# Performance work log

Hardware: AMD Instinct MI355X
Metric: run time of the kernel (lower is better)

## Reference

```python
import jax, jax.numpy as jnp
import numpy as np

B, T, E, H, R = 128, 64, 2048, 1024, 8  # batch, context_window, utter_hidden*2, user_dim, max_roles


def _gru_params(key, in_dim, hid):
    k1, k2, k3, k4 = jax.random.split(key, 4)
    s = 1.0 / np.sqrt(hid)
    return (jax.random.uniform(k1, (3 * hid, in_dim), jnp.float32, -s, s),
            jax.random.uniform(k2, (3 * hid, hid), jnp.float32, -s, s),
            jax.random.uniform(k3, (3 * hid,), jnp.float32, -s, s),
            jax.random.uniform(k4, (3 * hid,), jnp.float32, -s, s))


def setup_inputs() -> dict:
    key = jax.random.key(0)
    ks = jax.random.split(key, 8)
    encoder_hiddens = jax.random.normal(ks[0], (B, T, E), jnp.float32)
    spk = jax.random.randint(ks[1], (B, T), 0, R)
    adr = (spk + jax.random.randint(ks[2], (B, T), 1, R)) % R  # guarantee adr != spk
    dig_users = jnp.stack([spk, adr], axis=-1).astype(jnp.int32)  # [B,T,2]
    ws_ih, ws_hh, ws_bih, ws_bhh = _gru_params(ks[3], E + H, H)  # GRUS: input=[enc; adr_state]
    wa_ih, wa_hh, wa_bih, wa_bhh = _gru_params(ks[4], E + H, H)  # GRUA: input=[enc; spk_state]
    wo_ih, wo_hh, wo_bih, wo_bhh = _gru_params(ks[5], E, H)      # GRUO: input=enc
    return dict(encoder_hiddens=encoder_hiddens, dig_users=dig_users,
                ws_ih=ws_ih, ws_hh=ws_hh, ws_bih=ws_bih, ws_bhh=ws_bhh,
                wa_ih=wa_ih, wa_hh=wa_hh, wa_bih=wa_bih, wa_bhh=wa_bhh,
                wo_ih=wo_ih, wo_hh=wo_hh, wo_bih=wo_bih, wo_bhh=wo_bhh)


def _gru_cell(x, h, w_ih, w_hh, b_ih, b_hh):
    # standard torch.nn.GRUCell math; x: [..., in_dim], h: [..., H]
    gi = x @ w_ih.T + b_ih
    gh = h @ w_hh.T + b_hh
    ir, iz, ig = jnp.split(gi, 3, axis=-1)
    hr, hz, hg = jnp.split(gh, 3, axis=-1)
    r = jax.nn.sigmoid(ir + hr)
    z = jax.nn.sigmoid(iz + hz)
    n = jnp.tanh(ig + r * hg)
    return (1.0 - z) * n + z * h


def reference(encoder_hiddens, dig_users, ws_ih, ws_hh, ws_bih, ws_bhh,
              wa_ih, wa_hh, wa_bih, wa_bhh, wo_ih, wo_hh, wo_bih, wo_bhh):
    bidx = jnp.arange(B)
    roles = jnp.arange(R)

    def step(A, xs):
        enc_t, spk_t, adr_t = xs  # [B,E], [B], [B]
        # others: ascending role indices excluding spk and adr -> [B, R-2]
        is_other = (roles[None, :] != spk_t[:, None]) & (roles[None, :] != adr_t[:, None])
        others = jnp.argsort(jnp.logical_not(is_other).astype(jnp.int32), axis=-1, stable=True)[:, : R - 2]
        # gather current role states (all from pre-update A, as in the original)
        spk_v = A[bidx, spk_t]                    # [B,H]
        adr_v = A[bidx, adr_t]                    # [B,H]
        oth_v = A[bidx[:, None], others]          # [B,R-2,H]
        new_spk = _gru_cell(jnp.concatenate([enc_t, adr_v], -1), spk_v, ws_ih, ws_hh, ws_bih, ws_bhh)
        new_adr = _gru_cell(jnp.concatenate([enc_t, spk_v], -1), adr_v, wa_ih, wa_hh, wa_bih, wa_bhh)
        enc_b = jnp.broadcast_to(enc_t[:, None, :], (B, R - 2, E))
        new_oth = _gru_cell(enc_b, oth_v, wo_ih, wo_hh, wo_bih, wo_bhh)
        # scatter back (spk, adr, others indices are disjoint per batch row)
        A = A.at[bidx, spk_t].set(new_spk)
        A = A.at[bidx, adr_t].set(new_adr)
        A = A.at[bidx[:, None], others].set(new_oth)
        return A, None

    A0 = jnp.zeros((B, R, H), jnp.float32)
    xs = (jnp.swapaxes(encoder_hiddens, 0, 1),  # [T,B,E]
          jnp.swapaxes(dig_users[..., 0], 0, 1),
          jnp.swapaxes(dig_users[..., 1], 0, 1))
    A, _ = jax.lax.scan(step, A0, xs)
    return A
```

## Files before the change

kernel.cpp:

```cpp
#include <hip/hip_runtime.h>
#include <math.h>
#include <stdint.h>

static constexpr int B_ = 128;
static constexpr int T_ = 64;
static constexpr int E_ = 2048;
static constexpr int H_ = 1024;
static constexpr int R_ = 8;
static constexpr int H3_ = 3 * H_;

typedef unsigned short u16;
typedef __attribute__((ext_vector_type(8))) __bf16 bf16x8;
typedef __attribute__((ext_vector_type(4))) float f32x4;

__device__ __forceinline__ u16 f2bf(float f) {
    uint32_t x = __float_as_uint(f);
    x += 0x7fffu + ((x >> 16) & 1u);
    return (u16)(x >> 16);
}
__device__ __forceinline__ float bf2f(u16 u) {
    return __uint_as_float(((uint32_t)u) << 16);
}

__device__ __forceinline__ void async_cp16(const u16* g, u16* l) {
    auto* g1 = (const __attribute__((address_space(1))) u16*)g;
    auto* l3 = (__attribute__((address_space(3))) u16*)(uintptr_t)l;
    __builtin_amdgcn_global_load_lds((const __attribute__((address_space(1))) void*)g1,
                                     (__attribute__((address_space(3))) void*)l3,
                                     16, 0, 0);
}


__global__ __launch_bounds__(256) void zero_kernel(float* __restrict__ p, int n) {
    int i = blockIdx.x * 256 + threadIdx.x;
    if (i < n) p[i] = 0.0f;
}

__global__ __launch_bounds__(256) void conv_bf(
    const float* __restrict__ src, int src_ld, int col0, int cols,
    u16* __restrict__ dst, int total4)
{
    int i4 = blockIdx.x * 256 + threadIdx.x;
    if (i4 >= total4) return;
    int i = i4 * 4;
    int r = i / cols, c = i - r * cols;
    const float4 v = *(const float4*)(src + (size_t)r * src_ld + col0 + c);
    ushort4 o;
    o.x = f2bf(v.x); o.y = f2bf(v.y); o.z = f2bf(v.z); o.w = f2bf(v.w);
    *(ushort4*)(dst + i) = o;
}

__global__ __launch_bounds__(256) void mfma_p1f(
    const u16* __restrict__ X, int t0, int tcshift,
    const u16* __restrict__ W1,
    const float* __restrict__ bs, const float* __restrict__ ba,
    const float* __restrict__ bo,
    u16* __restrict__ GI, size_t GI_elems)
{
    __shared__ u16 As[2][128 * 64];
    __shared__ u16 Bs[2][128 * 64];
    const int tid = threadIdx.x;
    const int which = blockIdx.x / 24;
    const int n0 = (blockIdx.x % 24) * 128;
    const int m0 = blockIdx.y * 128;
    const int tcmask = (1 << tcshift) - 1;

    const u16* W = W1 + (size_t)which * H3_ * E_;
    const float* bias = (which == 0) ? bs : (which == 1) ? ba : bo;
    u16* C = GI + (size_t)which * GI_elems;

    const int lane = tid & 63;
    const int wm = ((tid >> 6) & 1) * 64;
    const int wn = (tid >> 7) * 64;
    const int fr = lane & 15;
    const int kq = (lane >> 4) * 8;
    const int ldsbase = (tid & 192) * 8;

    const int srow = tid >> 3;
    const int sce  = (((tid & 7) * 16) ^ ((srow & 7) << 4)) >> 1;

    f32x4 acc[4][4] = {};

    auto stage = [&](int buf, int k0) {
#pragma unroll
        for (int p = 0; p < 4; ++p) {
            int mrow = m0 + p * 32 + srow;
            int ro = ((mrow >> tcshift) * T_ + t0 + (mrow & tcmask)) * E_;
            async_cp16(X + ro + k0 + sce, &As[buf][p * 2048 + ldsbase]);
            int nrow = n0 + p * 32 + srow;
            async_cp16(W + (size_t)nrow * E_ + k0 + sce, &Bs[buf][p * 2048 + ldsbase]);
        }
    };
    auto compute = [&](int buf) {
#pragma unroll
        for (int kk = 0; kk < 2; ++kk) {
            bf16x8 a[4], b[4];
#pragma unroll
            for (int i = 0; i < 4; ++i) {
                int ra = wm + i * 16 + fr;
                int oa = (ra * 128 + kk * 64 + kq * 2) ^ ((ra & 7) << 4);
                a[i] = *(const bf16x8*)((const char*)&As[buf][0] + oa);
                int rb = wn + i * 16 + fr;
                int ob = (rb * 128 + kk * 64 + kq * 2) ^ ((rb & 7) << 4);
                b[i] = *(const bf16x8*)((const char*)&Bs[buf][0] + ob);
            }
#pragma unroll
            for (int mt = 0; mt < 4; ++mt)
#pragma unroll
                for (int nt = 0; nt < 4; ++nt)
                    acc[mt][nt] = __builtin_amdgcn_mfma_f32_16x16x32_bf16(
                        a[mt], b[nt], acc[mt][nt], 0, 0, 0);
        }
    };

    stage(0, 0);
    __syncthreads();
    int cur = 0;
    for (int k0 = 64; k0 < E_; k0 += 64) {
        stage(cur ^ 1, k0);
        compute(cur);
        __syncthreads();
        cur ^= 1;
    }
    compute(cur);

#pragma unroll
    for (int mt = 0; mt < 4; ++mt)
#pragma unroll
        for (int nt = 0; nt < 4; ++nt) {
            int n = n0 + wn + nt * 16 + fr;
            float bv = bias[n];
#pragma unroll
            for (int i = 0; i < 4; ++i) {
                int m = m0 + wm + mt * 16 + (lane >> 4) * 4 + i;
                C[(size_t)m * H3_ + n] = f2bf(acc[mt][nt][i] + bv);
            }
        }
}

__global__ __launch_bounds__(256) void mfma_step(
    const u16* __restrict__ Abf, const int* __restrict__ dig, int t,
    const u16* __restrict__ Whsi, const u16* __restrict__ Whs,
    const u16* __restrict__ Whai, const u16* __restrict__ Wha,
    const u16* __restrict__ Who, float* __restrict__ G)
{
    __shared__ u16 As[2][64 * 64];
    __shared__ u16 Bs[2][64 * 64];
    __shared__ int rowoff[64];
    const int tid = threadIdx.x;
    const int n0 = blockIdx.x * 64;
    const int row0 = blockIdx.y * 64;

    const u16* W;
    if      (row0 < 128) W = Whsi;
    else if (row0 < 256) W = Whs;
    else if (row0 < 384) W = Whai;
    else if (row0 < 512) W = Wha;
    else                 W = Who;

    if (tid < 64) {
        int mo = row0 + tid;
        int b, role;
        if (mo < 512) {
            b = mo & 127;
            int kind = mo >> 7;
            int spk = dig[(b * T_ + t) * 2 + 0];
            int adr = dig[(b * T_ + t) * 2 + 1];
            role = (kind == 0 || kind == 3) ? adr : spk;
        } else {
            int o = mo - 512;
            b = o / 6;
            int j = o - b * 6;
            int spk = dig[(b * T_ + t) * 2 + 0];
            int adr = dig[(b * T_ + t) * 2 + 1];
            int cnt = 0; role = 0;
            for (int r = 0; r < R_; ++r) {
                if (r != spk && r != adr) {
                    if (cnt == j) { role = r; break; }
                    ++cnt;
                }
            }
        }
        rowoff[tid] = (b * R_ + role) * H_;
    }
    __syncthreads();

    const int lane = tid & 63;
    const int wid = tid >> 6;
    const int wm = (wid & 1) * 32;
    const int wn = (wid >> 1) * 32;
    const int fr = lane & 15;
    const int kq = (lane >> 4) * 8;
    const int ldsbase = (tid & 192) * 8;

    const int srow = tid >> 3;
    const int sce  = (((tid & 7) * 16) ^ ((srow & 7) << 4)) >> 1;

    f32x4 acc[2][2] = {};

    auto stage = [&](int buf, int k0) {
#pragma unroll
        for (int p = 0; p < 2; ++p) {
            int r = p * 32 + srow;
            async_cp16(Abf + rowoff[r] + k0 + sce, &As[buf][p * 2048 + ldsbase]);
            async_cp16(W + (size_t)(n0 + r) * H_ + k0 + sce, &Bs[buf][p * 2048 + ldsbase]);
        }
    };
    auto compute = [&](int buf) {
#pragma unroll
        for (int kk = 0; kk < 2; ++kk) {
            bf16x8 a[2], b[2];
#pragma unroll
            for (int i = 0; i < 2; ++i) {
                int ra = wm + i * 16 + fr;
                int oa = (ra * 128 + kk * 64 + kq * 2) ^ ((ra & 7) << 4);
                a[i] = *(const bf16x8*)((const char*)&As[buf][0] + oa);
                int rb = wn + i * 16 + fr;
                int ob = (rb * 128 + kk * 64 + kq * 2) ^ ((rb & 7) << 4);
                b[i] = *(const bf16x8*)((const char*)&Bs[buf][0] + ob);
            }
#pragma unroll
            for (int mt = 0; mt < 2; ++mt)
#pragma unroll
                for (int nt = 0; nt < 2; ++nt)
                    acc[mt][nt] = __builtin_amdgcn_mfma_f32_16x16x32_bf16(
                        a[mt], b[nt], acc[mt][nt], 0, 0, 0);
        }
    };

    stage(0, 0);
    __syncthreads();
    int cur = 0;
    for (int k0 = 64; k0 < H_; k0 += 64) {
        stage(cur ^ 1, k0);
        compute(cur);
        __syncthreads();
        cur ^= 1;
    }
    compute(cur);

#pragma unroll
    for (int mt = 0; mt < 2; ++mt)
#pragma unroll
        for (int nt = 0; nt < 2; ++nt) {
            int n = n0 + wn + nt * 16 + fr;
#pragma unroll
            for (int i = 0; i < 4; ++i) {
                int mo = row0 + wm + mt * 16 + (lane >> 4) * 4 + i;
                G[(size_t)mo * H3_ + n] = acc[mt][nt][i];
            }
        }
}

__global__ __launch_bounds__(256) void gate_kernel(
    const float* __restrict__ Aold, float* __restrict__ Anew,
    u16* __restrict__ Abf,
    const int* __restrict__ dig, int t, int tloc, int Tc,
    const u16* __restrict__ GIX, const u16* __restrict__ GIA,
    const u16* __restrict__ GIO, const float* __restrict__ G,
    const float* __restrict__ ws_bhh, const float* __restrict__ wa_bhh,
    const float* __restrict__ wo_bhh)
{
    const int blk = blockIdx.x;
    const int b = blk >> 3, r = blk & 7;
    const int spk = dig[(b * T_ + t) * 2 + 0];
    const int adr = dig[(b * T_ + t) * 2 + 1];
    const size_t gi_row = (size_t)(b * Tc + tloc) * H3_;

    const u16* gi_pre;
    const float* gi_add;
    const float* gh;
    const float* bhh;
    if (r == spk) {
        gi_pre = GIX + gi_row;
        gi_add = G + (size_t)b * H3_;
        gh     = G + (size_t)(128 + b) * H3_;
        bhh    = ws_bhh;
    } else if (r == adr) {
        gi_pre = GIA + gi_row;
        gi_add = G + (size_t)(256 + b) * H3_;
        gh     = G + (size_t)(384 + b) * H3_;
        bhh    = wa_bhh;
    } else {
        int oidx = r - (spk < r ? 1 : 0) - (adr < r ? 1 : 0);
        gi_pre = GIO + gi_row;
        gi_add = nullptr;
        gh     = G + (size_t)(512 + b * 6 + oidx) * H3_;
        bhh    = wo_bhh;
    }

    const size_t hoff = (size_t)(b * R_ + r) * H_;
    for (int i = threadIdx.x; i < H_; i += 256) {
        float gir = bf2f(gi_pre[i]);
        float giz = bf2f(gi_pre[H_ + i]);
        float gin = bf2f(gi_pre[2 * H_ + i]);
        if (gi_add) {
            gir += gi_add[i];
            giz += gi_add[H_ + i];
            gin += gi_add[2 * H_ + i];
        }
        float ghr = gh[i]          + bhh[i];
        float ghz = gh[H_ + i]     + bhh[H_ + i];
        float ghn = gh[2 * H_ + i] + bhh[2 * H_ + i];

        float rg = 1.0f / (1.0f + __expf(-(gir + ghr)));
        float zg = 1.0f / (1.0f + __expf(-(giz + ghz)));
        float ng = tanhf(gin + rg * ghn);
        float h  = Aold[hoff + i];
        float o  = (1.0f - zg) * ng + zg * h;
        Anew[hoff + i] = o;
        Abf[hoff + i]  = f2bf(o);
    }
}

extern "C" void kernel_launch(void* const* d_in, const int* in_sizes, int n_in,
                              void* d_out, int out_size, void* d_ws, size_t ws_size,
                              hipStream_t stream) {
    const float* enc    = (const float*)d_in[0];
    const int*   dig    = (const int*)d_in[1];
    const float* ws_ih  = (const float*)d_in[2];
    const float* ws_hh  = (const float*)d_in[3];
    const float* ws_bih = (const float*)d_in[4];
    const float* ws_bhh = (const float*)d_in[5];
    const float* wa_ih  = (const float*)d_in[6];
    const float* wa_hh  = (const float*)d_in[7];
    const float* wa_bih = (const float*)d_in[8];
    const float* wa_bhh = (const float*)d_in[9];
    const float* wo_ih  = (const float*)d_in[10];
    const float* wo_hh  = (const float*)d_in[11];
    const float* wo_bih = (const float*)d_in[12];
    const float* wo_bhh = (const float*)d_in[13];

    float* A0 = (float*)d_out;

    char* p = (char*)d_ws;
    auto take = [&](size_t bytes) { char* q = p; p += (bytes + 255) & ~(size_t)255; return q; };
    u16*   enc_bf = (u16*)  take((size_t)B_ * T_ * E_ * 2);
    u16*   W1     = (u16*)  take((size_t)3 * H3_ * E_ * 2);
    u16*   W1s    = W1;
    u16*   W1a    = W1 + (size_t)H3_ * E_;
    u16*   W1o    = W1a + (size_t)H3_ * E_;
    u16*   Whsi   = (u16*)  take((size_t)H3_ * H_ * 2);
    u16*   Whai   = (u16*)  take((size_t)H3_ * H_ * 2);
    u16*   Whs    = (u16*)  take((size_t)H3_ * H_ * 2);
    u16*   Wha    = (u16*)  take((size_t)H3_ * H_ * 2);
    u16*   Who    = (u16*)  take((size_t)H3_ * H_ * 2);
    u16*   Abf    = (u16*)  take((size_t)B_ * R_ * H_ * 2);
    float* A1     = (float*)take((size_t)B_ * R_ * H_ * 4);
    float* G      = (float*)take((size_t)1280 * H3_ * 4);
    size_t fixed = (size_t)(p - (char*)d_ws);

    const size_t per_t = (size_t)3 * B_ * H3_ * 2;
    int Tc = 64;
    while (Tc > 1 && fixed + per_t * (size_t)Tc > ws_size) Tc >>= 1;
    int tcshift = 0;
    while ((1 << tcshift) < Tc) ++tcshift;
    const size_t GI_elems = (size_t)B_ * Tc * H3_;
    u16* GI  = (u16*)take(3 * GI_elems * 2);
    u16* GIX = GI;
    u16* GIA = GI + GI_elems;
    u16* GIO = GIA + GI_elems;

    dim3 blk(256);
    const size_t A_sz = (size_t)B_ * R_ * H_;

    zero_kernel<<<dim3((int)((A_sz + 255) / 256)), blk, 0, stream>>>(A0, (int)A_sz);
    zero_kernel<<<dim3((int)((A_sz / 2 + 255) / 256)), blk, 0, stream>>>((float*)Abf, (int)(A_sz / 2));

    {
        int t4;
        t4 = B_ * T_ * E_ / 4;
        conv_bf<<<dim3((t4 + 255) / 256), blk, 0, stream>>>(enc, E_, 0, E_, enc_bf, t4);
        t4 = H3_ * E_ / 4;
        conv_bf<<<dim3((t4 + 255) / 256), blk, 0, stream>>>(ws_ih, E_ + H_, 0, E_, W1s, t4);
        conv_bf<<<dim3((t4 + 255) / 256), blk, 0, stream>>>(wa_ih, E_ + H_, 0, E_, W1a, t4);
        conv_bf<<<dim3((t4 + 255) / 256), blk, 0, stream>>>(wo_ih, E_, 0, E_, W1o, t4);
        t4 = H3_ * H_ / 4;
        conv_bf<<<dim3((t4 + 255) / 256), blk, 0, stream>>>(ws_ih, E_ + H_, E_, H_, Whsi, t4);
        conv_bf<<<dim3((t4 + 255) / 256), blk, 0, stream>>>(wa_ih, E_ + H_, E_, H_, Whai, t4);
        conv_bf<<<dim3((t4 + 255) / 256), blk, 0, stream>>>(ws_hh, H_, 0, H_, Whs, t4);
        conv_bf<<<dim3((t4 + 255) / 256), blk, 0, stream>>>(wa_hh, H_, 0, H_, Wha, t4);
        conv_bf<<<dim3((t4 + 255) / 256), blk, 0, stream>>>(wo_hh, H_, 0, H_, Who, t4);
    }

    float* Aold = A0;
    float* Anew = A1;
    for (int t0 = 0; t0 < T_; t0 += Tc) {
        dim3 g1(72, (B_ * Tc) / 128);
        mfma_p1f<<<g1, blk, 0, stream>>>(enc_bf, t0, tcshift, W1,
                                         ws_bih, wa_bih, wo_bih, GI, GI_elems);

        for (int t = t0; t < t0 + Tc; ++t) {
            mfma_step<<<dim3(48, 20), blk, 0, stream>>>(
                Abf, dig, t, Whsi, Whs, Whai, Wha, Who, G);
            gate_kernel<<<dim3(B_ * R_), blk, 0, stream>>>(
                Aold, Anew, Abf, dig, t, t - t0, Tc, GIX, GIA, GIO, G,
                ws_bhh, wa_bhh, wo_bhh);
            float* tmp = Aold; Aold = Anew; Anew = tmp;
        }
    }
}
```

Measured before the change: 2.168 ms.

## Enlarge step GEMM M-tile with XCD-aware block mapping, vectorize gate kernel

The per-step recurrent GEMM now uses 128-row M tiles instead of 64, so each block reuses one loaded weight tile across twice as many rows, and the grid is halved. Blocks are remapped so that blocks sharing the same weight group land on the same XCD, aiming for better L2 locality. The input-projection GEMM swaps grid axes so consecutive blocks share weight tiles, and its bf16 output is written with nontemporal stores. The gate kernel is vectorized to four elements per thread with float4 loads, dropping the strided loop. These add register pressure and rely on H equalling four times the block size.

```diff
diff --git a/kernel.cpp b/kernel.cpp
--- a/kernel.cpp
+++ b/kernel.cpp
@@ -10,6 +10,7 @@
 static constexpr int H3_ = 3 * H_;
 
 typedef unsigned short u16;
+typedef __attribute__((ext_vector_type(4))) unsigned short u16x4;
 typedef __attribute__((ext_vector_type(8))) __bf16 bf16x8;
 typedef __attribute__((ext_vector_type(4))) float f32x4;
 
@@ -60,9 +61,9 @@
     __shared__ u16 As[2][128 * 64];
     __shared__ u16 Bs[2][128 * 64];
     const int tid = threadIdx.x;
-    const int which = blockIdx.x / 24;
-    const int n0 = (blockIdx.x % 24) * 128;
-    const int m0 = blockIdx.y * 128;
+    const int m0 = blockIdx.x * 128;
+    const int which = blockIdx.y / 24;
+    const int n0 = (blockIdx.y % 24) * 128;
     const int tcmask = (1 << tcshift) - 1;
 
     const u16* W = W1 + (size_t)which * H3_ * E_;
@@ -133,7 +134,8 @@
 #pragma unroll
             for (int i = 0; i < 4; ++i) {
                 int m = m0 + wm + mt * 16 + (lane >> 4) * 4 + i;
-                C[(size_t)m * H3_ + n] = f2bf(acc[mt][nt][i] + bv);
+                __builtin_nontemporal_store(f2bf(acc[mt][nt][i] + bv),
+                                            &C[(size_t)m * H3_ + n]);
             }
         }
 }
@@ -144,21 +146,32 @@
     const u16* __restrict__ Whai, const u16* __restrict__ Wha,
     const u16* __restrict__ Who, float* __restrict__ G)
 {
-    __shared__ u16 As[2][64 * 64];
+    __shared__ u16 As[2][128 * 64];
     __shared__ u16 Bs[2][64 * 64];
-    __shared__ int rowoff[64];
+    __shared__ int rowoff[128];
     const int tid = threadIdx.x;
-    const int n0 = blockIdx.x * 64;
-    const int row0 = blockIdx.y * 64;
+
+    const int wgid = blockIdx.y * 48 + blockIdx.x;
+    const int xcd = wgid & 7;
+    const int slot = wgid >> 3;
+    int g, n0i;
+    if (slot < 48) { g = xcd; n0i = slot; }
+    else {
+        int s = slot - 48;
+        g = 8 + (xcd >> 2);
+        n0i = s * 4 + (xcd & 3);
+    }
+    const int row0 = g * 128;
+    const int n0 = n0i * 64;
 
     const u16* W;
-    if      (row0 < 128) W = Whsi;
-    else if (row0 < 256) W = Whs;
-    else if (row0 < 384) W = Whai;
-    else if (row0 < 512) W = Wha;
-    else                 W = Who;
-
-    if (tid < 64) {
+    if      (g == 0) W = Whsi;
+    else if (g == 1) W = Whs;
+    else if (g == 2) W = Whai;
+    else if (g == 3) W = Wha;
+    else             W = Who;
+
+    if (tid < 128) {
         int mo = row0 + tid;
         int b, role;
         if (mo < 512) {
@@ -187,7 +200,7 @@
 
     const int lane = tid & 63;
     const int wid = tid >> 6;
-    const int wm = (wid & 1) * 32;
+    const int wm = (wid & 1) * 64;
     const int wn = (wid >> 1) * 32;
     const int fr = lane & 15;
     const int kq = (lane >> 4) * 8;
@@ -196,31 +209,38 @@
     const int srow = tid >> 3;
     const int sce  = (((tid & 7) * 16) ^ ((srow & 7) << 4)) >> 1;
 
-    f32x4 acc[2][2] = {};
+    f32x4 acc[4][2] = {};
 
     auto stage = [&](int buf, int k0) {
+#pragma unroll
+        for (int p = 0; p < 4; ++p) {
+            int r = p * 32 + srow;
+            async_cp16(Abf + rowoff[r] + k0 + sce, &As[buf][p * 2048 + ldsbase]);
+        }
 #pragma unroll
         for (int p = 0; p < 2; ++p) {
             int r = p * 32 + srow;
-            async_cp16(Abf + rowoff[r] + k0 + sce, &As[buf][p * 2048 + ldsbase]);
             async_cp16(W + (size_t)(n0 + r) * H_ + k0 + sce, &Bs[buf][p * 2048 + ldsbase]);
         }
     };
     auto compute = [&](int buf) {
 #pragma unroll
         for (int kk = 0; kk < 2; ++kk) {
-            bf16x8 a[2], b[2];
-#pragma unroll
-            for (int i = 0; i < 2; ++i) {
+            bf16x8 a[4], b[2];
+#pragma unroll
+            for (int i = 0; i < 4; ++i) {
                 int ra = wm + i * 16 + fr;
                 int oa = (ra * 128 + kk * 64 + kq * 2) ^ ((ra & 7) << 4);
                 a[i] = *(const bf16x8*)((const char*)&As[buf][0] + oa);
-                int rb = wn + i * 16 + fr;
+            }
+#pragma unroll
+            for (int j = 0; j < 2; ++j) {
+                int rb = wn + j * 16 + fr;
                 int ob = (rb * 128 + kk * 64 + kq * 2) ^ ((rb & 7) << 4);
-                b[i] = *(const bf16x8*)((const char*)&Bs[buf][0] + ob);
-            }
-#pragma unroll
-            for (int mt = 0; mt < 2; ++mt)
+                b[j] = *(const bf16x8*)((const char*)&Bs[buf][0] + ob);
+            }
+#pragma unroll
+            for (int mt = 0; mt < 4; ++mt)
 #pragma unroll
                 for (int nt = 0; nt < 2; ++nt)
                     acc[mt][nt] = __builtin_amdgcn_mfma_f32_16x16x32_bf16(
@@ -240,7 +260,7 @@
     compute(cur);
 
 #pragma unroll
-    for (int mt = 0; mt < 2; ++mt)
+    for (int mt = 0; mt < 4; ++mt)
 #pragma unroll
         for (int nt = 0; nt < 2; ++nt) {
             int n = n0 + wn + nt * 16 + fr;
@@ -290,27 +310,55 @@
     }
 
     const size_t hoff = (size_t)(b * R_ + r) * H_;
-    for (int i = threadIdx.x; i < H_; i += 256) {
-        float gir = bf2f(gi_pre[i]);
-        float giz = bf2f(gi_pre[H_ + i]);
-        float gin = bf2f(gi_pre[2 * H_ + i]);
-        if (gi_add) {
-            gir += gi_add[i];
-            giz += gi_add[H_ + i];
-            gin += gi_add[2 * H_ + i];
-        }
-        float ghr = gh[i]          + bhh[i];
-        float ghz = gh[H_ + i]     + bhh[H_ + i];
-        float ghn = gh[2 * H_ + i] + bhh[2 * H_ + i];
-
-        float rg = 1.0f / (1.0f + __expf(-(gir + ghr)));
-        float zg = 1.0f / (1.0f + __expf(-(giz + ghz)));
-        float ng = tanhf(gin + rg * ghn);
-        float h  = Aold[hoff + i];
-        float o  = (1.0f - zg) * ng + zg * h;
-        Anew[hoff + i] = o;
-        Abf[hoff + i]  = f2bf(o);
-    }
+    const int i0 = threadIdx.x * 4;
+    float gir[4], giz[4], gin[4];
+    {
+        const u16x4 pr = __builtin_nontemporal_load((const u16x4*)(gi_pre + i0));
+        const u16x4 pz = __builtin_nontemporal_load((const u16x4*)(gi_pre + H_ + i0));
+        const u16x4 pn = __builtin_nontemporal_load((const u16x4*)(gi_pre + 2 * H_ + i0));
+#pragma unroll
+        for (int j = 0; j < 4; ++j) {
+            gir[j] = bf2f(pr[j]);
+            giz[j] = bf2f(pz[j]);
+            gin[j] = bf2f(pn[j]);
+        }
+    }
+    if (gi_add) {
+        const float4 ar = *(const float4*)(gi_add + i0);
+        const float4 az = *(const float4*)(gi_add + H_ + i0);
+        const float4 an = *(const float4*)(gi_add + 2 * H_ + i0);
+        gir[0] += ar.x; gir[1] += ar.y; gir[2] += ar.z; gir[3] += ar.w;
+        giz[0] += az.x; giz[1] += az.y; giz[2] += az.z; giz[3] += az.w;
+        gin[0] += an.x; gin[1] += an.y; gin[2] += an.z; gin[3] += an.w;
+    }
+    const float4 hr4 = *(const float4*)(gh + i0);
+    const float4 hz4 = *(const float4*)(gh + H_ + i0);
+    const float4 hn4 = *(const float4*)(gh + 2 * H_ + i0);
+    const float4 br4 = *(const float4*)(bhh + i0);
+    const float4 bz4 = *(const float4*)(bhh + H_ + i0);
+    const float4 bn4 = *(const float4*)(bhh + 2 * H_ + i0);
+    const float4 h4  = *(const float4*)(Aold + hoff + i0);
+
+    float ghr[4] = {hr4.x + br4.x, hr4.y + br4.y, hr4.z + br4.z, hr4.w + br4.w};
+    float ghz[4] = {hz4.x + bz4.x, hz4.y + bz4.y, hz4.z + bz4.z, hz4.w + bz4.w};
+    float ghn[4] = {hn4.x + bn4.x, hn4.y + bn4.y, hn4.z + bn4.z, hn4.w + bn4.w};
+    float hold[4] = {h4.x, h4.y, h4.z, h4.w};
+
+    float4 o4;
+    ushort4 ob4;
+    float* op = &o4.x;
+    u16* obp = &ob4.x;
+#pragma unroll
+    for (int j = 0; j < 4; ++j) {
+        float rg = 1.0f / (1.0f + __expf(-(gir[j] + ghr[j])));
+        float zg = 1.0f / (1.0f + __expf(-(giz[j] + ghz[j])));
+        float ng = tanhf(gin[j] + rg * ghn[j]);
+        float o  = (1.0f - zg) * ng + zg * hold[j];
+        op[j] = o;
+        obp[j] = f2bf(o);
+    }
+    *(float4*)(Anew + hoff + i0) = o4;
+    *(ushort4*)(Abf + hoff + i0) = ob4;
 }
 
 extern "C" void kernel_launch(void* const* d_in, const int* in_sizes, int n_in,
@@ -386,12 +434,12 @@
     float* Aold = A0;
     float* Anew = A1;
     for (int t0 = 0; t0 < T_; t0 += Tc) {
-        dim3 g1(72, (B_ * Tc) / 128);
+        dim3 g1((B_ * Tc) / 128, 72);
         mfma_p1f<<<g1, blk, 0, stream>>>(enc_bf, t0, tcshift, W1,
                                          ws_bih, wa_bih, wo_bih, GI, GI_elems);
 
         for (int t = t0; t < t0 + Tc; ++t) {
-            mfma_step<<<dim3(48, 20), blk, 0, stream>>>(
+            mfma_step<<<dim3(48, 10), blk, 0, stream>>>(
                 Abf, dig, t, Whsi, Whs, Whai, Wha, Who, G);
             gate_kernel<<<dim3(B_ * R_), blk, 0, stream>>>(
                 Aold, Anew, Abf, dig, t, t - t0, Tc, GIX, GIA, GIO, G,
```

Measured after the change: 2.174 ms. Within noise of the previous version (+0.3%).

## Fuse per-step recurrent GEMM with GRU gate epilogue into single kernel

Applied to the files above, without the earlier changes.

Merges the per-timestep recurrent matmul and the gate kernel into one launch. Each block computes all three gate column slices for a 64-column chunk, so the GRU update can be applied directly from the accumulators instead of round-tripping through a float G buffer. The bf16 state is double-buffered so the in-place read/write hazard goes away, and blocks are mapped with XCD-aware indexing. The input-projection GEMM grid is also transposed. The trade-offs are larger LDS use per block, divergent heavy/light blocks, and fewer but larger (512-thread) workgroups per step.

```diff
diff --git a/kernel.cpp b/kernel.cpp
--- a/kernel.cpp
+++ b/kernel.cpp
@@ -60,9 +60,9 @@
     __shared__ u16 As[2][128 * 64];
     __shared__ u16 Bs[2][128 * 64];
     const int tid = threadIdx.x;
-    const int which = blockIdx.x / 24;
-    const int n0 = (blockIdx.x % 24) * 128;
-    const int m0 = blockIdx.y * 128;
+    const int m0 = blockIdx.x * 128;
+    const int which = blockIdx.y / 24;
+    const int n0 = (blockIdx.y % 24) * 128;
     const int tcmask = (1 << tcshift) - 1;
 
     const u16* W = W1 + (size_t)which * H3_ * E_;
@@ -138,93 +138,119 @@
         }
 }
 
-__global__ __launch_bounds__(256) void mfma_step(
-    const u16* __restrict__ Abf, const int* __restrict__ dig, int t,
+__global__ __launch_bounds__(512) void step_fused(
+    const u16* __restrict__ Abf_old, u16* __restrict__ Abf_new,
+    const float* __restrict__ Aold, float* __restrict__ Anew,
+    const int* __restrict__ dig, int t, int tloc, int Tc,
     const u16* __restrict__ Whsi, const u16* __restrict__ Whs,
     const u16* __restrict__ Whai, const u16* __restrict__ Wha,
-    const u16* __restrict__ Who, float* __restrict__ G)
+    const u16* __restrict__ Who,
+    const u16* __restrict__ GIX, const u16* __restrict__ GIA,
+    const u16* __restrict__ GIO,
+    const float* __restrict__ ws_bhh, const float* __restrict__ wa_bhh,
+    const float* __restrict__ wo_bhh)
 {
-    __shared__ u16 As[2][64 * 64];
-    __shared__ u16 Bs[2][64 * 64];
-    __shared__ int rowoff[64];
+    __shared__ u16 Bs1[2][192 * 64];
+    __shared__ u16 Bs2[2][192 * 64];
+    __shared__ u16 As1[2][64 * 64];
+    __shared__ u16 As2[2][64 * 64];
+    __shared__ int roffA1[64], roffA2[64], bIdx[64];
+
     const int tid = threadIdx.x;
-    const int n0 = blockIdx.x * 64;
-    const int row0 = blockIdx.y * 64;
-
-    const u16* W;
-    if      (row0 < 128) W = Whsi;
-    else if (row0 < 256) W = Whs;
-    else if (row0 < 384) W = Whai;
-    else if (row0 < 512) W = Wha;
-    else                 W = Who;
+    const int wgid = blockIdx.x;
+    const int xcd = wgid & 7;
+    const int slot = wgid >> 3;
+    const int cb = (slot >> 4) * 8 + xcd;
+    const int ty = slot & 15;
+    const int c0 = cb * 64;
+
+    const bool heavy = (ty < 4);
+    const u16 *WB1, *WB2 = nullptr;
+    const u16* GIsrc;
+    const float* bhh;
+    int b0 = 0, o0 = 0;
+    if (ty < 2)      { b0 = ty * 64;       WB1 = Whsi; WB2 = Whs; GIsrc = GIX; bhh = ws_bhh; }
+    else if (ty < 4) { b0 = (ty - 2) * 64; WB1 = Whai; WB2 = Wha; GIsrc = GIA; bhh = wa_bhh; }
+    else             { o0 = (ty - 4) * 64; WB1 = Who;             GIsrc = GIO; bhh = wo_bhh; }
 
     if (tid < 64) {
-        int mo = row0 + tid;
-        int b, role;
-        if (mo < 512) {
-            b = mo & 127;
-            int kind = mo >> 7;
+        if (heavy) {
+            int b = b0 + tid;
             int spk = dig[(b * T_ + t) * 2 + 0];
             int adr = dig[(b * T_ + t) * 2 + 1];
-            role = (kind == 0 || kind == 3) ? adr : spk;
+            int own = (ty < 2) ? spk : adr;
+            int oth = (ty < 2) ? adr : spk;
+            roffA1[tid] = (b * R_ + oth) * H_;
+            roffA2[tid] = (b * R_ + own) * H_;
+            bIdx[tid] = b;
         } else {
-            int o = mo - 512;
-            b = o / 6;
-            int j = o - b * 6;
+            int mo = o0 + tid;
+            int b = mo / 6, j = mo - b * 6;
             int spk = dig[(b * T_ + t) * 2 + 0];
             int adr = dig[(b * T_ + t) * 2 + 1];
-            int cnt = 0; role = 0;
-            for (int r = 0; r < R_; ++r) {
-                if (r != spk && r != adr) {
-                    if (cnt == j) { role = r; break; }
-                    ++cnt;
-                }
-            }
-        }
-        rowoff[tid] = (b * R_ + role) * H_;
+            int cnt = 0, role = 0;
+            for (int r = 0; r < R_; ++r)
+                if (r != spk && r != adr) { if (cnt == j) { role = r; break; } ++cnt; }
+            roffA1[tid] = (b * R_ + role) * H_;
+            bIdx[tid] = b;
+        }
     }
     __syncthreads();
 
     const int lane = tid & 63;
     const int wid = tid >> 6;
-    const int wm = (wid & 1) * 32;
-    const int wn = (wid >> 1) * 32;
-    const int fr = lane & 15;
-    const int kq = (lane >> 4) * 8;
-    const int ldsbase = (tid & 192) * 8;
+    const int m0w = (wid >> 2) * 32;
+    const int w   = wid & 3;
+    const int fr  = lane & 15;
+    const int kq  = (lane >> 4) * 8;
 
     const int srow = tid >> 3;
     const int sce  = (((tid & 7) * 16) ^ ((srow & 7) << 4)) >> 1;
-
-    f32x4 acc[2][2] = {};
+    const int ldsA = (tid & 448) * 8;
+
+    f32x4 acc1[3][2] = {};
+    f32x4 acc2[3][2] = {};
 
     auto stage = [&](int buf, int k0) {
-#pragma unroll
-        for (int p = 0; p < 2; ++p) {
-            int r = p * 32 + srow;
-            async_cp16(Abf + rowoff[r] + k0 + sce, &As[buf][p * 2048 + ldsbase]);
-            async_cp16(W + (size_t)(n0 + r) * H_ + k0 + sce, &Bs[buf][p * 2048 + ldsbase]);
+        async_cp16(Abf_old + roffA1[srow] + k0 + sce, &As1[buf][ldsA]);
+        if (heavy)
+            async_cp16(Abf_old + roffA2[srow] + k0 + sce, &As2[buf][ldsA]);
+#pragma unroll
+        for (int p = 0; p < 3; ++p) {
+            int wr = c0 + p * H_ + srow;
+            async_cp16(WB1 + (size_t)wr * H_ + k0 + sce, &Bs1[buf][p * 4096 + ldsA]);
+            if (heavy)
+                async_cp16(WB2 + (size_t)wr * H_ + k0 + sce, &Bs2[buf][p * 4096 + ldsA]);
         }
     };
     auto compute = [&](int buf) {
 #pragma unroll
         for (int kk = 0; kk < 2; ++kk) {
-            bf16x8 a[2], b[2];
+            bf16x8 a1[2], a2[2], b1[3], b2[3];
 #pragma unroll
             for (int i = 0; i < 2; ++i) {
-                int ra = wm + i * 16 + fr;
-                int oa = (ra * 128 + kk * 64 + kq * 2) ^ ((ra & 7) << 4);
-                a[i] = *(const bf16x8*)((const char*)&As[buf][0] + oa);
-                int rb = wn + i * 16 + fr;
-                int ob = (rb * 128 + kk * 64 + kq * 2) ^ ((rb & 7) << 4);
-                b[i] = *(const bf16x8*)((const char*)&Bs[buf][0] + ob);
-            }
-#pragma unroll
-            for (int mt = 0; mt < 2; ++mt)
-#pragma unroll
-                for (int nt = 0; nt < 2; ++nt)
-                    acc[mt][nt] = __builtin_amdgcn_mfma_f32_16x16x32_bf16(
-                        a[mt], b[nt], acc[mt][nt], 0, 0, 0);
+                int r = m0w + i * 16 + fr;
+                int off = (r * 128 + kk * 64 + kq * 2) ^ ((r & 7) << 4);
+                a1[i] = *(const bf16x8*)((const char*)&As1[buf][0] + off);
+                if (heavy) a2[i] = *(const bf16x8*)((const char*)&As2[buf][0] + off);
+            }
+#pragma unroll
+            for (int g = 0; g < 3; ++g) {
+                int r = g * 64 + w * 16 + fr;
+                int off = (r * 128 + kk * 64 + kq * 2) ^ ((r & 7) << 4);
+                b1[g] = *(const bf16x8*)((const char*)&Bs1[buf][0] + off);
+                if (heavy) b2[g] = *(const bf16x8*)((const char*)&Bs2[buf][0] + off);
+            }
+#pragma unroll
+            for (int g = 0; g < 3; ++g)
+#pragma unroll
+                for (int i = 0; i < 2; ++i) {
+                    acc1[g][i] = __builtin_amdgcn_mfma_f32_16x16x32_bf16(
+                        a1[i], b1[g], acc1[g][i], 0, 0, 0);
+                    if (heavy)
+                        acc2[g][i] = __builtin_amdgcn_mfma_f32_16x16x32_bf16(
+                            a2[i], b2[g], acc2[g][i], 0, 0, 0);
+                }
         }
     };
 
@@ -239,77 +265,42 @@
     }
     compute(cur);
 
-#pragma unroll
-    for (int mt = 0; mt < 2; ++mt)
-#pragma unroll
-        for (int nt = 0; nt < 2; ++nt) {
-            int n = n0 + wn + nt * 16 + fr;
-#pragma unroll
-            for (int i = 0; i < 4; ++i) {
-                int mo = row0 + wm + mt * 16 + (lane >> 4) * 4 + i;
-                G[(size_t)mo * H3_ + n] = acc[mt][nt][i];
-            }
-        }
-}
-
-__global__ __launch_bounds__(256) void gate_kernel(
-    const float* __restrict__ Aold, float* __restrict__ Anew,
-    u16* __restrict__ Abf,
-    const int* __restrict__ dig, int t, int tloc, int Tc,
-    const u16* __restrict__ GIX, const u16* __restrict__ GIA,
-    const u16* __restrict__ GIO, const float* __restrict__ G,
-    const float* __restrict__ ws_bhh, const float* __restrict__ wa_bhh,
-    const float* __restrict__ wo_bhh)
-{
-    const int blk = blockIdx.x;
-    const int b = blk >> 3, r = blk & 7;
-    const int spk = dig[(b * T_ + t) * 2 + 0];
-    const int adr = dig[(b * T_ + t) * 2 + 1];
-    const size_t gi_row = (size_t)(b * Tc + tloc) * H3_;
-
-    const u16* gi_pre;
-    const float* gi_add;
-    const float* gh;
-    const float* bhh;
-    if (r == spk) {
-        gi_pre = GIX + gi_row;
-        gi_add = G + (size_t)b * H3_;
-        gh     = G + (size_t)(128 + b) * H3_;
-        bhh    = ws_bhh;
-    } else if (r == adr) {
-        gi_pre = GIA + gi_row;
-        gi_add = G + (size_t)(256 + b) * H3_;
-        gh     = G + (size_t)(384 + b) * H3_;
-        bhh    = wa_bhh;
-    } else {
-        int oidx = r - (spk < r ? 1 : 0) - (adr < r ? 1 : 0);
-        gi_pre = GIO + gi_row;
-        gi_add = nullptr;
-        gh     = G + (size_t)(512 + b * 6 + oidx) * H3_;
-        bhh    = wo_bhh;
-    }
-
-    const size_t hoff = (size_t)(b * R_ + r) * H_;
-    for (int i = threadIdx.x; i < H_; i += 256) {
-        float gir = bf2f(gi_pre[i]);
-        float giz = bf2f(gi_pre[H_ + i]);
-        float gin = bf2f(gi_pre[2 * H_ + i]);
-        if (gi_add) {
-            gir += gi_add[i];
-            giz += gi_add[H_ + i];
-            gin += gi_add[2 * H_ + i];
-        }
-        float ghr = gh[i]          + bhh[i];
-        float ghz = gh[H_ + i]     + bhh[H_ + i];
-        float ghn = gh[2 * H_ + i] + bhh[2 * H_ + i];
-
-        float rg = 1.0f / (1.0f + __expf(-(gir + ghr)));
-        float zg = 1.0f / (1.0f + __expf(-(giz + ghz)));
-        float ng = tanhf(gin + rg * ghn);
-        float h  = Aold[hoff + i];
-        float o  = (1.0f - zg) * ng + zg * h;
-        Anew[hoff + i] = o;
-        Abf[hoff + i]  = f2bf(o);
+    const int col = c0 + w * 16 + fr;
+    const float bh_r = bhh[col];
+    const float bh_z = bhh[H_ + col];
+    const float bh_n = bhh[2 * H_ + col];
+#pragma unroll
+    for (int mt = 0; mt < 2; ++mt) {
+#pragma unroll
+        for (int i = 0; i < 4; ++i) {
+            int lr = m0w + mt * 16 + (lane >> 4) * 4 + i;
+            int b  = bIdx[lr];
+            size_t girow = (size_t)(b * Tc + tloc) * H3_;
+            float gir = bf2f(GIsrc[girow + col]);
+            float giz = bf2f(GIsrc[girow + H_ + col]);
+            float gin = bf2f(GIsrc[girow + 2 * H_ + col]);
+            float ghr, ghz, ghn;
+            if (heavy) {
+                gir += acc1[0][mt][i];
+                giz += acc1[1][mt][i];
+                gin += acc1[2][mt][i];
+                ghr = acc2[0][mt][i] + bh_r;
+                ghz = acc2[1][mt][i] + bh_z;
+                ghn = acc2[2][mt][i] + bh_n;
+            } else {
+                ghr = acc1[0][mt][i] + bh_r;
+                ghz = acc1[1][mt][i] + bh_z;
+                ghn = acc1[2][mt][i] + bh_n;
+            }
+            int ooff = heavy ? roffA2[lr] : roffA1[lr];
+            float rg = 1.0f / (1.0f + __expf(-(gir + ghr)));
+            float zg = 1.0f / (1.0f + __expf(-(giz + ghz)));
+            float ng = tanhf(gin + rg * ghn);
+            float h  = Aold[ooff + col];
+            float o  = (1.0f - zg) * ng + zg * h;
+            Anew[ooff + col] = o;
+            Abf_new[ooff + col] = f2bf(o);
+        }
     }
 }
 
@@ -345,9 +336,9 @@
     u16*   Whs    = (u16*)  take((size_t)H3_ * H_ * 2);
     u16*   Wha    = (u16*)  take((size_t)H3_ * H_ * 2);
     u16*   Who    = (u16*)  take((size_t)H3_ * H_ * 2);
-    u16*   Abf    = (u16*)  take((size_t)B_ * R_ * H_ * 2);
+    u16*   AbfA   = (u16*)  take((size_t)B_ * R_ * H_ * 2);
+    u16*   AbfB   = (u16*)  take((size_t)B_ * R_ * H_ * 2);
     float* A1     = (float*)take((size_t)B_ * R_ * H_ * 4);
-    float* G      = (float*)take((size_t)1280 * H3_ * 4);
     size_t fixed = (size_t)(p - (char*)d_ws);
 
     const size_t per_t = (size_t)3 * B_ * H3_ * 2;
@@ -365,7 +356,7 @@
     const size_t A_sz = (size_t)B_ * R_ * H_;
 
     zero_kernel<<<dim3((int)((A_sz + 255) / 256)), blk, 0, stream>>>(A0, (int)A_sz);
-    zero_kernel<<<dim3((int)((A_sz / 2 + 255) / 256)), blk, 0, stream>>>((float*)Abf, (int)(A_sz / 2));
+    zero_kernel<<<dim3((int)((A_sz / 2 + 255) / 256)), blk, 0, stream>>>((float*)AbfA, (int)(A_sz / 2));
 
     {
         int t4;
@@ -385,18 +376,20 @@
 
     float* Aold = A0;
     float* Anew = A1;
+    u16* AbfOld = AbfA;
+    u16* AbfNew = AbfB;
     for (int t0 = 0; t0 < T_; t0 += Tc) {
-        dim3 g1(72, (B_ * Tc) / 128);
+        dim3 g1((B_ * Tc) / 128, 72);
         mfma_p1f<<<g1, blk, 0, stream>>>(enc_bf, t0, tcshift, W1,
                                          ws_bih, wa_bih, wo_bih, GI, GI_elems);
 
         for (int t = t0; t < t0 + Tc; ++t) {
-            mfma_step<<<dim3(48, 20), blk, 0, stream>>>(
-                Abf, dig, t, Whsi, Whs, Whai, Wha, Who, G);
-            gate_kernel<<<dim3(B_ * R_), blk, 0, stream>>>(
-                Aold, Anew, Abf, dig, t, t - t0, Tc, GIX, GIA, GIO, G,
+            step_fused<<<dim3(256), dim3(512), 0, stream>>>(
+                AbfOld, AbfNew, Aold, Anew, dig, t, t - t0, Tc,
+                Whsi, Whs, Whai, Wha, Who, GIX, GIA, GIO,
                 ws_bhh, wa_bhh, wo_bhh);
-            float* tmp = Aold; Aold = Anew; Anew = tmp;
-        }
-    }
-}
+            float* tf = Aold; Aold = Anew; Anew = tf;
+            u16* tb = AbfOld; AbfOld = AbfNew; AbfNew = tb;
+        }
+    }
+}
```

Measured after the change: 2.198 ms. Within noise of the previous version (+1.4%).
